# Optimization experiments

Hardware: AMD Instinct MI355X
Metric: run time of the kernel (lower is better)

## Reference

```python
import jax, jax.numpy as jnp
import numpy as np

B, C, N1 = 8, 1, 255
C_HID = 8
N2 = 2 * (N1 + 1)          # 512: antisymmetric expansion size
CROP = 2 * (N2 // 4) + 1   # 257: spectral crop size


def _expand(r):
    # odd antisymmetric extension to size 2*(M+1) x 2*(N+1)
    b, c, m, n = r.shape
    rsym = jnp.zeros((b, c, 2 * (m + 1), 2 * (n + 1)), r.dtype)
    rsym = rsym.at[:, :, 1:m + 1, 1:n + 1].set(r)
    rsym = rsym.at[:, :, m + 2:, 1:n + 1].set(-r[:, :, ::-1, :])
    rsym = rsym.at[:, :, 1:m + 1, n + 2:].set(-r[:, :, :, ::-1])
    rsym = rsym.at[:, :, m + 2:, n + 2:].set(r[:, :, ::-1, ::-1])
    return rsym


def _per_sample_conv(x, w):
    # Per-sample 3x3 cross-correlation, padding=1.
    # Equivalent to the torch module's F.conv2d over flattened [B*Cout,Cin,3,3]
    # followed by batch-diagonal extraction (without the O(B) wasted cross terms).
    # x: [B, Cin, H, W] complex; w: [B, Cout, Cin, 3, 3] complex.
    h, wd = x.shape[-2], x.shape[-1]
    xp = jnp.pad(x, ((0, 0), (0, 0), (1, 1), (1, 1)))
    out = 0.
    for di in range(3):
        for dj in range(3):
            out = out + jnp.einsum('bchw,boc->bohw', xp[:, :, di:di + h, dj:dj + wd], w[:, :, :, di, dj])
    return out


def _wT(w):
    # torch: transpose(-4,-3).transpose(-2,-1).conj() on [B,Cout,Cin,kh,kw]
    return jnp.conj(jnp.swapaxes(jnp.swapaxes(w, 1, 2), -2, -1))


def _forward(r, w1, w2, w3, theta):
    n1 = r.shape[-1]
    rsym = _expand(r)
    n2 = rsym.shape[-1]
    pl = n2 // 4 + 1
    pr = n2 - n2 // 2 - pl
    rh = jnp.fft.fftshift(jnp.fft.ifft2(rsym, axes=(2, 3)), axes=(2, 3))
    lo, hi = n2 // 2 - n2 // 4, n2 // 2 + n2 // 4 + 1
    rh = rh[:, :, lo:hi, lo:hi]                     # [B, C, CROP, CROP] complex
    for w in (w1, w2, w3):
        rh = _per_sample_conv(rh, w)
    out = rh * theta                                # spectral diagonal multiply
    for w in (_wT(w3), _wT(w2), _wT(w1)):
        out = _per_sample_conv(out, w)
    out = jnp.pad(out, ((0, 0), (0, 0), (pl, pr), (pl, pr)))
    out = jnp.fft.ifftshift(out, axes=(2, 3))
    e = jnp.fft.fft2(out, axes=(2, 3))
    return e[:, :, :n1, :n1]


def setup_inputs():
    key = jax.random.key(0)
    ks = jax.random.split(key, 9)
    s = jnp.float32(0.1)
    return {
        'r': jax.random.normal(ks[0], (B, C, N1, N1), jnp.float32),
        'w1_re': s * jax.random.normal(ks[1], (B, C_HID, C, 3, 3), jnp.float32),
        'w1_im': s * jax.random.normal(ks[2], (B, C_HID, C, 3, 3), jnp.float32),
        'w2_re': s * jax.random.normal(ks[3], (B, C_HID, C_HID, 3, 3), jnp.float32),
        'w2_im': s * jax.random.normal(ks[4], (B, C_HID, C_HID, 3, 3), jnp.float32),
        'w3_re': s * jax.random.normal(ks[5], (B, C_HID, C_HID, 3, 3), jnp.float32),
        'w3_im': s * jax.random.normal(ks[6], (B, C_HID, C_HID, 3, 3), jnp.float32),
        'theta_re': s * jax.random.normal(ks[7], (B, C_HID, CROP, CROP), jnp.float32),
        'theta_im': s * jax.random.normal(ks[8], (B, C_HID, CROP, CROP), jnp.float32),
    }


def reference(r, w1_re, w1_im, w2_re, w2_im, w3_re, w3_im, theta_re, theta_im):
    w1 = w1_re + 1j * w1_im
    w2 = w2_re + 1j * w2_im
    w3 = w3_re + 1j * w3_im
    theta = theta_re + 1j * theta_im
    return _forward(r, w1, w2, w3, theta)
```

## Files before the change

kernel.cpp:

```cpp
#include <hip/hip_runtime.h>

#define NB 8
#define CH 8
#define N1S 255
#define CROP 257
#define NOUT 255
#define CC (CROP * CROP)

static constexpr float PI2 = 6.28318530717958647692f;

__device__ inline unsigned short f2bf(float f) {
  unsigned int u = __float_as_uint(f);
  unsigned int lsb = (u >> 16) & 1u;
  u += 0x7fffu + lsb;
  return (unsigned short)(u >> 16);
}

__global__ void k_fill(unsigned short* __restrict__ out, int n, float v) {
  int i = blockIdx.x * 256 + threadIdx.x;
  if (i < n) out[i] = f2bf(v);
}

__global__ void k_tables(float* __restrict__ T, float* __restrict__ Tt,
                         float2* __restrict__ D, float2* __restrict__ Dt) {
  int idx = blockIdx.x * blockDim.x + threadIdx.x;
  if (idx < CROP * N1S) {
    int a = idx / N1S, p = idx % N1S;
    int v = (p + 1) * (a - 128);
    int t = v % 512; if (t < 0) t += 512; if (t >= 256) t -= 512;
    float s = sinf((float)t * (PI2 / 512.0f));
    T[a * N1S + p] = s;
    Tt[p * CROP + a] = s;
  }
  if (idx < NOUT * CROP) {
    int k = idx / CROP, j = idx % CROP;
    int v = k * (j - 127);
    int t = v % 513; if (t < 0) t += 513; if (t > 256) t -= 513;
    float ang = (float)t * (PI2 / 513.0f);
    float2 d = make_float2(cosf(ang), -sinf(ang));
    D[k * CROP + j] = d;
    Dt[j * NOUT + k] = d;
  }
}

__global__ void k_wprep(const float* __restrict__ w1re, const float* __restrict__ w1im,
                        const float* __restrict__ w2re, const float* __restrict__ w2im,
                        const float* __restrict__ w3re, const float* __restrict__ w3im,
                        float* __restrict__ wp) {
  int p = blockIdx.x * 256 + threadIdx.x;
  if (p >= 19584) return;
  int l, off;
  if      (p < 576)   { l = 0; off = 0; }
  else if (p < 5184)  { l = 1; off = 576; }
  else if (p < 9792)  { l = 2; off = 5184; }
  else if (p < 14400) { l = 3; off = 9792; }
  else if (p < 19008) { l = 4; off = 14400; }
  else                { l = 5; off = 19008; }
  int q = p - off;
  int cin  = (l == 0) ? 1 : 8;
  int cout = (l == 5) ? 1 : 8;
  int per_b = cin * cout * 9;
  int b = q / per_b, rem = q % per_b;
  int c = rem / (cout * 9), rem2 = rem % (cout * 9);
  int o = rem2 / 9, t9 = rem2 % 9;
  int di = t9 / 3, dj = t9 % 3;
  const float *wre, *wim;
  if (l == 0 || l == 5) { wre = w1re; wim = w1im; }
  else if (l == 1 || l == 4) { wre = w2re; wim = w2im; }
  else { wre = w3re; wim = w3im; }
  bool trans = (l >= 3);
  float wr, wi;
  if (trans) {
    int widx = (((b * cin + c) * cout + o) * 3 + dj) * 3 + di;
    wr = wre[widx]; wi = -wim[widx];
  } else {
    int widx = (((b * cout + o) * cin + c) * 3 + di) * 3 + dj;
    wr = wre[widx]; wi = wim[widx];
  }
  wp[2 * p] = wr;
  wp[2 * p + 1] = wi;
}


__global__ __launch_bounds__(512) void k_dst1(const float* __restrict__ r,
                                              const float* __restrict__ T,
                                              float* __restrict__ tmp) {
  __shared__ float As[32][16];
  __shared__ float Bs[16][64];
  const int tx = threadIdx.x, ty = threadIdx.y;
  const int tid = ty * 64 + tx;
  const int b = blockIdx.z;
  const int n = blockIdx.x * 64 + tx;
  const int a_base = blockIdx.y * 32;
  const float* rb = r + (size_t)b * N1S * N1S;
  float acc[4] = {};
  for (int mc = 0; mc < N1S; mc += 16) {
    { int row = tid / 16, col = tid % 16;
      int a = a_base + row, m = mc + col;
      As[row][col] = (a < CROP && m < N1S) ? T[a * N1S + m] : 0.f; }
    { int row = tid / 64, col = tid % 64;
      #pragma unroll
      for (int rr = 0; rr < 2; ++rr) {
        int m = mc + row + rr * 8, nn = blockIdx.x * 64 + col;
        Bs[row + rr * 8][col] = (m < N1S && nn < N1S) ? rb[m * N1S + nn] : 0.f;
      } }
    __syncthreads();
    #pragma unroll
    for (int jj = 0; jj < 16; ++jj) {
      float x = Bs[jj][tx];
      #pragma unroll
      for (int q = 0; q < 4; ++q)
        acc[q] = fmaf(As[ty * 4 + q][jj], x, acc[q]);
    }
    __syncthreads();
  }
  if (n < N1S) {
    #pragma unroll
    for (int q = 0; q < 4; ++q) {
      int a = a_base + ty * 4 + q;
      if (a < CROP) tmp[((size_t)b * CROP + a) * N1S + n] = acc[q];
    }
  }
}

__global__ __launch_bounds__(512) void k_dst2(const float* __restrict__ tmp,
                                              const float* __restrict__ Tt,
                                              float2* __restrict__ z0) {
  __shared__ float As[32][16];
  __shared__ float Bs[16][64];
  const int tx = threadIdx.x, ty = threadIdx.y;
  const int tid = ty * 64 + tx;
  const int b = blockIdx.z;
  const int a2 = blockIdx.x * 64 + tx;
  const int a_base = blockIdx.y * 32;
  const float* tb = tmp + (size_t)b * CROP * N1S;
  float acc[4] = {};
  for (int nc = 0; nc < N1S; nc += 16) {
    { int row = tid / 16, col = tid % 16;
      int a1 = a_base + row, nn = nc + col;
      As[row][col] = (a1 < CROP && nn < N1S) ? tb[a1 * N1S + nn] : 0.f; }
    { int row = tid / 64, col = tid % 64;
      #pragma unroll
      for (int rr = 0; rr < 2; ++rr) {
        int nn = nc + row + rr * 8, aa2 = blockIdx.x * 64 + col;
        Bs[row + rr * 8][col] = (nn < N1S && aa2 < CROP) ? Tt[nn * CROP + aa2] : 0.f;
      } }
    __syncthreads();
    #pragma unroll
    for (int jj = 0; jj < 16; ++jj) {
      float x = Bs[jj][tx];
      #pragma unroll
      for (int q = 0; q < 4; ++q)
        acc[q] = fmaf(As[ty * 4 + q][jj], x, acc[q]);
    }
    __syncthreads();
  }
  if (a2 < CROP) {
    #pragma unroll
    for (int q = 0; q < 4; ++q) {
      int a1 = a_base + ty * 4 + q;
      if (a1 < CROP)
        z0[((size_t)b * CROP + a1) * CROP + a2] = make_float2(acc[q] * (-1.0f / 65536.0f), 0.f);
    }
  }
}

__global__ __launch_bounds__(512) void k_f1(const float2* __restrict__ z,
                                            const float2* __restrict__ D,
                                            float2* __restrict__ t) {
  __shared__ float2 As[32][16];
  __shared__ float2 Bs[16][64];
  const int tx = threadIdx.x, ty = threadIdx.y;
  const int tid = ty * 64 + tx;
  const int b = blockIdx.z;
  const int j2 = blockIdx.x * 64 + tx;
  const int k_base = blockIdx.y * 32;
  const float2* zb = z + (size_t)b * CC;
  float tr[4] = {}, ti[4] = {};
  for (int jc = 0; jc < CROP; jc += 16) {
    { int row = tid / 16, col = tid % 16;
      int k = k_base + row, j1 = jc + col;
      As[row][col] = (k < NOUT && j1 < CROP) ? D[k * CROP + j1] : make_float2(0.f, 0.f); }
    { int row = tid / 64, col = tid % 64;
      #pragma unroll
      for (int rr = 0; rr < 2; ++rr) {
        int j1 = jc + row + rr * 8, jj2 = blockIdx.x * 64 + col;
        Bs[row + rr * 8][col] = (j1 < CROP && jj2 < CROP) ? zb[j1 * CROP + jj2] : make_float2(0.f, 0.f);
      } }
    __syncthreads();
    #pragma unroll
    for (int jj = 0; jj < 16; ++jj) {
      float2 zv = Bs[jj][tx];
      #pragma unroll
      for (int q = 0; q < 4; ++q) {
        float2 d = As[ty * 4 + q][jj];
        tr[q] = fmaf(d.x, zv.x, tr[q]); tr[q] = fmaf(-d.y, zv.y, tr[q]);
        ti[q] = fmaf(d.x, zv.y, ti[q]); ti[q] = fmaf(d.y, zv.x, ti[q]);
      }
    }
    __syncthreads();
  }
  if (j2 < CROP) {
    #pragma unroll
    for (int q = 0; q < 4; ++q) {
      int k = k_base + ty * 4 + q;
      if (k < NOUT)
        t[((size_t)b * NOUT + k) * CROP + j2] = make_float2(tr[q], ti[q]);
    }
  }
}

__global__ __launch_bounds__(512) void k_f2(const float2* __restrict__ t,
                                            const float2* __restrict__ Dt,
                                            ushort2* __restrict__ out) {
  __shared__ float2 As[32][16];
  __shared__ float2 Bs[16][64];
  const int tx = threadIdx.x, ty = threadIdx.y;
  const int tid = ty * 64 + tx;
  const int b = blockIdx.z;
  const int k2 = blockIdx.x * 64 + tx;
  const int k_base = blockIdx.y * 32;
  const float2* tb = t + (size_t)b * NOUT * CROP;
  float er[4] = {}, ei[4] = {};
  for (int jc = 0; jc < CROP; jc += 16) {
    { int row = tid / 16, col = tid % 16;
      int k1 = k_base + row, j = jc + col;
      As[row][col] = (k1 < NOUT && j < CROP) ? tb[k1 * CROP + j] : make_float2(0.f, 0.f); }
    { int row = tid / 64, col = tid % 64;
      #pragma unroll
      for (int rr = 0; rr < 2; ++rr) {
        int j = jc + row + rr * 8, kk2 = blockIdx.x * 64 + col;
        Bs[row + rr * 8][col] = (j < CROP && kk2 < NOUT) ? Dt[j * NOUT + kk2] : make_float2(0.f, 0.f);
      } }
    __syncthreads();
    #pragma unroll
    for (int jj = 0; jj < 16; ++jj) {
      float2 dv = Bs[jj][tx];
      #pragma unroll
      for (int q = 0; q < 4; ++q) {
        float2 tv = As[ty * 4 + q][jj];
        er[q] = fmaf(tv.x, dv.x, er[q]); er[q] = fmaf(-tv.y, dv.y, er[q]);
        ei[q] = fmaf(tv.x, dv.y, ei[q]); ei[q] = fmaf(tv.y, dv.x, ei[q]);
      }
    }
    __syncthreads();
  }
  if (k2 < NOUT) {
    #pragma unroll
    for (int q = 0; q < 4; ++q) {
      int k1 = k_base + ty * 4 + q;
      if (k1 < NOUT)
        out[((size_t)b * NOUT + k1) * NOUT + k2] = make_ushort2(f2bf(ei[q]), f2bf(er[q]));
    }
  }
}

template<int CIN, int COUT, bool THETA, bool REALIN>
__global__ __launch_bounds__(256) void k_conv(const float2* __restrict__ in,
                                              const float* __restrict__ wl,
                                              const float* __restrict__ tre,
                                              const float* __restrict__ tim,
                                              float2* __restrict__ out) {
  __shared__ float2 tile[CIN][18][18];
  const int b = blockIdx.z;
  const int tx = threadIdx.x, ty = threadIdx.y;
  const int tid = ty * 16 + tx;
  const int ox0 = blockIdx.x * 16, oy0 = blockIdx.y * 16;

  const float2* inb = in + (size_t)b * CIN * CC;
  for (int c = 0; c < CIN; ++c) {
    for (int idx = tid; idx < 18 * 18; idx += 256) {
      int iy = idx / 18, ix = idx % 18;
      int gy = oy0 + iy - 1, gx = ox0 + ix - 1;
      float2 v = make_float2(0.f, 0.f);
      if (gy >= 0 && gy < CROP && gx >= 0 && gx < CROP)
        v = inb[(c * CROP + gy) * CROP + gx];
      tile[c][iy][ix] = v;
    }
  }
  __syncthreads();
  const int ox = ox0 + tx, oy = oy0 + ty;
  if (ox >= CROP || oy >= CROP) return;
  float accr[COUT], acci[COUT];
  #pragma unroll
  for (int o = 0; o < COUT; ++o) { accr[o] = 0.f; acci[o] = 0.f; }
  #pragma unroll 1
  for (int c = 0; c < CIN; ++c) {
    const float* wsc = wl + (size_t)2 * ((b * CIN + c) * COUT * 9);
    float xr[9], xi[9];
    #pragma unroll
    for (int t9 = 0; t9 < 9; ++t9) {
      float2 v = tile[c][ty + t9 / 3][tx + t9 % 3];
      xr[t9] = v.x; if (!REALIN) xi[t9] = v.y;
    }
    #pragma unroll
    for (int o = 0; o < COUT; ++o) {
      #pragma unroll
      for (int t9 = 0; t9 < 9; ++t9) {
        float wr = wsc[(o * 9 + t9) * 2];
        float wi = wsc[(o * 9 + t9) * 2 + 1];
        if (REALIN) {
          accr[o] = fmaf(wr, xr[t9], accr[o]);
          acci[o] = fmaf(wi, xr[t9], acci[o]);
        } else {
          accr[o] = fmaf(wr, xr[t9], accr[o]);
          accr[o] = fmaf(-wi, xi[t9], accr[o]);
          acci[o] = fmaf(wr, xi[t9], acci[o]);
          acci[o] = fmaf(wi, xr[t9], acci[o]);
        }
      }
    }
  }
  float2* outb = out + (size_t)b * COUT * CC;
  #pragma unroll
  for (int o = 0; o < COUT; ++o) {
    float orv = accr[o], oiv = acci[o];
    if (THETA) {
      size_t tix = ((size_t)(b * COUT + o) * CROP + oy) * CROP + ox;
      float trv = tre[tix], tiv = tim[tix];
      float nr = orv * trv - oiv * tiv;
      float ni = orv * tiv + oiv * trv;
      orv = nr; oiv = ni;
    }
    outb[(o * CROP + oy) * CROP + ox] = make_float2(orv, oiv);
  }
}

extern "C" void kernel_launch(void* const* d_in, const int* in_sizes, int n_in,
                              void* d_out, int out_size, void* d_ws, size_t ws_size,
                              hipStream_t stream) {
  (void)ws_size;
  static const int EXP[9] = {520200, 576, 576, 4608, 4608, 4608, 4608, 4227136, 4227136};
  int bad = -1;
  if (n_in != 9) bad = 90;
  else for (int i = 0; i < 9; ++i) if (in_sizes[i] != EXP[i]) { bad = i; break; }
  if (bad >= 0) {
    float v = (bad == 90) ? 99.0f : (100.0f + (float)bad);
    k_fill<<<(out_size + 255) / 256, 256, 0, stream>>>((unsigned short*)d_out, out_size, v);
    return;
  }

  const float* r    = (const float*)d_in[0];
  const float* w1re = (const float*)d_in[1];
  const float* w1im = (const float*)d_in[2];
  const float* w2re = (const float*)d_in[3];
  const float* w2im = (const float*)d_in[4];
  const float* w3re = (const float*)d_in[5];
  const float* w3im = (const float*)d_in[6];
  const float* thre = (const float*)d_in[7];
  const float* thim = (const float*)d_in[8];

  float* ws = (float*)d_ws;
  size_t off = 0;
  auto alloc = [&](size_t n) { float* p = ws + off; off += (n + 63) & ~(size_t)63; return p; };
  float*  T    = alloc((size_t)CROP * N1S);
  float*  Tt   = alloc((size_t)N1S * CROP);
  float2* D    = (float2*)alloc((size_t)NOUT * CROP * 2);
  float2* Dt   = (float2*)alloc((size_t)CROP * NOUT * 2);
  float*  wp   = alloc((size_t)2 * 19584);
  float*  tmpA = alloc((size_t)NB * CROP * N1S);
  float2* z0   = (float2*)alloc((size_t)NB * CC * 2);
  float2* tmpF = (float2*)alloc((size_t)NB * NOUT * CROP * 2);
  float2* A    = (float2*)alloc((size_t)NB * CH * CC * 2);
  float2* Bb   = (float2*)alloc((size_t)NB * CH * CC * 2);

  k_tables<<<dim3((CROP * N1S + 255) / 256), dim3(256), 0, stream>>>(T, Tt, D, Dt);
  k_wprep<<<dim3(77), dim3(256), 0, stream>>>(w1re, w1im, w2re, w2im, w3re, w3im, wp);
  k_dst1<<<dim3(4, 9, NB), dim3(64, 8), 0, stream>>>(r, T, tmpA);
  k_dst2<<<dim3(5, 9, NB), dim3(64, 8), 0, stream>>>(tmpA, Tt, z0);

  dim3 cgrid(17, 17, NB), cblk(16, 16);
  k_conv<1, 8, false, true ><<<cgrid, cblk, 0, stream>>>(z0, wp + 2 * 0,     nullptr, nullptr, A);
  k_conv<8, 8, false, false><<<cgrid, cblk, 0, stream>>>(A,  wp + 2 * 576,   nullptr, nullptr, Bb);
  k_conv<8, 8, true , false><<<cgrid, cblk, 0, stream>>>(Bb, wp + 2 * 5184,  thre, thim, A);
  k_conv<8, 8, false, false><<<cgrid, cblk, 0, stream>>>(A,  wp + 2 * 9792,  nullptr, nullptr, Bb);
  k_conv<8, 8, false, false><<<cgrid, cblk, 0, stream>>>(Bb, wp + 2 * 14400, nullptr, nullptr, A);
  k_conv<8, 1, false, false><<<cgrid, cblk, 0, stream>>>(A,  wp + 2 * 19008, nullptr, nullptr, z0);

  k_f1<<<dim3(5, 8, NB), dim3(64, 8), 0, stream>>>(z0, D, tmpF);
  k_f2<<<dim3(4, 8, NB), dim3(64, 8), 0, stream>>>(tmpF, Dt, (ushort2*)d_out);
}
```

Measured before the change: 335.3 us.

## Fuse consecutive 3x3 complex convolutions pairwise with halo recompute in shared memory

Replaces six separate per-sample conv launches with three fused kernels, each running two 3x3 convolutions back to back. The intermediate 16x16 tile, which carries a one-pixel halo, stays in shared memory, and the theta multiply is applied between the two convs of the middle pair. This removes three global round-trips of the 8-channel complex intermediate and three launches. In exchange, each block now produces only 14x14 outputs, so halo work is recomputed and more blocks are launched. Shared memory use per block also goes up.

```diff
diff --git a/kernel.cpp b/kernel.cpp
--- a/kernel.cpp
+++ b/kernel.cpp
@@ -255,74 +255,115 @@
   }
 }
 
-template<int CIN, int COUT, bool THETA, bool REALIN>
-__global__ __launch_bounds__(256) void k_conv(const float2* __restrict__ in,
-                                              const float* __restrict__ wl,
-                                              const float* __restrict__ tre,
-                                              const float* __restrict__ tim,
-                                              float2* __restrict__ out) {
-  __shared__ float2 tile[CIN][18][18];
+template<int CIN, int COUT2, bool THETA_MID, bool REALIN>
+__global__ __launch_bounds__(256) void k_fused(const float2* __restrict__ in,
+                                               const float* __restrict__ wlA,
+                                               const float* __restrict__ wlB,
+                                               const float* __restrict__ tre,
+                                               const float* __restrict__ tim,
+                                               float2* __restrict__ out) {
+  __shared__ float2 tile1[CIN][18][18];
+  __shared__ float2 mid[8][16][17];
   const int b = blockIdx.z;
   const int tx = threadIdx.x, ty = threadIdx.y;
   const int tid = ty * 16 + tx;
-  const int ox0 = blockIdx.x * 16, oy0 = blockIdx.y * 16;
+  const int ox0 = blockIdx.x * 14, oy0 = blockIdx.y * 14;
 
   const float2* inb = in + (size_t)b * CIN * CC;
-  for (int c = 0; c < CIN; ++c) {
-    for (int idx = tid; idx < 18 * 18; idx += 256) {
-      int iy = idx / 18, ix = idx % 18;
-      int gy = oy0 + iy - 1, gx = ox0 + ix - 1;
-      float2 v = make_float2(0.f, 0.f);
-      if (gy >= 0 && gy < CROP && gx >= 0 && gx < CROP)
-        v = inb[(c * CROP + gy) * CROP + gx];
-      tile[c][iy][ix] = v;
-    }
+  #pragma unroll 1
+  for (int idx = tid; idx < CIN * 18 * 18; idx += 256) {
+    int c = idx / (18 * 18), rem = idx % (18 * 18);
+    int iy = rem / 18, ix = rem % 18;
+    int gy = oy0 + iy - 2, gx = ox0 + ix - 2;
+    float2 v = make_float2(0.f, 0.f);
+    if (gy >= 0 && gy < CROP && gx >= 0 && gx < CROP)
+      v = inb[(c * CROP + gy) * CROP + gx];
+    tile1[c][iy][ix] = v;
   }
   __syncthreads();
-  const int ox = ox0 + tx, oy = oy0 + ty;
-  if (ox >= CROP || oy >= CROP) return;
-  float accr[COUT], acci[COUT];
-  #pragma unroll
-  for (int o = 0; o < COUT; ++o) { accr[o] = 0.f; acci[o] = 0.f; }
-  #pragma unroll 1
-  for (int c = 0; c < CIN; ++c) {
-    const float* wsc = wl + (size_t)2 * ((b * CIN + c) * COUT * 9);
-    float xr[9], xi[9];
-    #pragma unroll
-    for (int t9 = 0; t9 < 9; ++t9) {
-      float2 v = tile[c][ty + t9 / 3][tx + t9 % 3];
-      xr[t9] = v.x; if (!REALIN) xi[t9] = v.y;
-    }
-    #pragma unroll
-    for (int o = 0; o < COUT; ++o) {
+
+  {
+    const int gmy = oy0 - 1 + ty, gmx = ox0 - 1 + tx;
+    const bool inside = (gmy >= 0 && gmy < CROP && gmx >= 0 && gmx < CROP);
+    float ar[8], ai[8];
+    #pragma unroll
+    for (int o = 0; o < 8; ++o) { ar[o] = 0.f; ai[o] = 0.f; }
+    #pragma unroll 1
+    for (int c = 0; c < CIN; ++c) {
+      const float* wsc = wlA + (size_t)2 * ((b * CIN + c) * 8 * 9);
+      float xr[9], xi[9];
       #pragma unroll
       for (int t9 = 0; t9 < 9; ++t9) {
-        float wr = wsc[(o * 9 + t9) * 2];
-        float wi = wsc[(o * 9 + t9) * 2 + 1];
-        if (REALIN) {
-          accr[o] = fmaf(wr, xr[t9], accr[o]);
-          acci[o] = fmaf(wi, xr[t9], acci[o]);
-        } else {
-          accr[o] = fmaf(wr, xr[t9], accr[o]);
-          accr[o] = fmaf(-wi, xi[t9], accr[o]);
-          acci[o] = fmaf(wr, xi[t9], acci[o]);
-          acci[o] = fmaf(wi, xr[t9], acci[o]);
+        float2 v = tile1[c][ty + t9 / 3][tx + t9 % 3];
+        xr[t9] = v.x; if (!REALIN) xi[t9] = v.y;
+      }
+      #pragma unroll
+      for (int o = 0; o < 8; ++o) {
+        #pragma unroll
+        for (int t9 = 0; t9 < 9; ++t9) {
+          float wr = wsc[(o * 9 + t9) * 2];
+          float wi = wsc[(o * 9 + t9) * 2 + 1];
+          if (REALIN) {
+            ar[o] = fmaf(wr, xr[t9], ar[o]);
+            ai[o] = fmaf(wi, xr[t9], ai[o]);
+          } else {
+            ar[o] = fmaf(wr, xr[t9], ar[o]);
+            ar[o] = fmaf(-wi, xi[t9], ar[o]);
+            ai[o] = fmaf(wr, xi[t9], ai[o]);
+            ai[o] = fmaf(wi, xr[t9], ai[o]);
+          }
         }
       }
     }
-  }
-  float2* outb = out + (size_t)b * COUT * CC;
-  #pragma unroll
-  for (int o = 0; o < COUT; ++o) {
-    float orv = accr[o], oiv = acci[o];
-    if (THETA) {
-      size_t tix = ((size_t)(b * COUT + o) * CROP + oy) * CROP + ox;
-      float trv = tre[tix], tiv = tim[tix];
-      float nr = orv * trv - oiv * tiv;
-      float ni = orv * tiv + oiv * trv;
-      orv = nr; oiv = ni;
-    }
-    outb[(o * CROP + oy) * CROP + ox] = make_float2(orv, oiv);
+    #pragma unroll
+    for (int o = 0; o < 8; ++o) {
+      float rv = ar[o], iv = ai[o];
+      if (THETA_MID) {
+        if (inside) {
+          size_t tix = ((size_t)(b * 8 + o) * CROP + gmy) * CROP + gmx;
+          float trv = tre[tix], tiv = tim[tix];
+          float nr = rv * trv - iv * tiv, ni = rv * tiv + iv * trv;
+          rv = nr; iv = ni;
+        }
+      }
+      mid[o][ty][tx] = inside ? make_float2(rv, iv) : make_float2(0.f, 0.f);
+    }
+  }
+  __syncthreads();
+
+  if (tx < 14 && ty < 14) {
+    const int oy = oy0 + ty, ox = ox0 + tx;
+    if (oy < CROP && ox < CROP) {
+      float ar[COUT2], ai[COUT2];
+      #pragma unroll
+      for (int o = 0; o < COUT2; ++o) { ar[o] = 0.f; ai[o] = 0.f; }
+      #pragma unroll 1
+      for (int c = 0; c < 8; ++c) {
+        const float* wsc = wlB + (size_t)2 * ((b * 8 + c) * COUT2 * 9);
+        float xr[9], xi[9];
+        #pragma unroll
+        for (int t9 = 0; t9 < 9; ++t9) {
+          float2 v = mid[c][ty + t9 / 3][tx + t9 % 3];
+          xr[t9] = v.x; xi[t9] = v.y;
+        }
+        #pragma unroll
+        for (int o = 0; o < COUT2; ++o) {
+          #pragma unroll
+          for (int t9 = 0; t9 < 9; ++t9) {
+            float wr = wsc[(o * 9 + t9) * 2];
+            float wi = wsc[(o * 9 + t9) * 2 + 1];
+            ar[o] = fmaf(wr, xr[t9], ar[o]);
+            ar[o] = fmaf(-wi, xi[t9], ar[o]);
+            ai[o] = fmaf(wr, xi[t9], ai[o]);
+            ai[o] = fmaf(wi, xr[t9], ai[o]);
+          }
+        }
+      }
+      float2* outb = out + (size_t)b * COUT2 * CC;
+      #pragma unroll
+      for (int o = 0; o < COUT2; ++o)
+        outb[(o * CROP + oy) * CROP + ox] = make_float2(ar[o], ai[o]);
+    }
   }
 }
 
@@ -369,13 +410,10 @@
   k_dst1<<<dim3(4, 9, NB), dim3(64, 8), 0, stream>>>(r, T, tmpA);
   k_dst2<<<dim3(5, 9, NB), dim3(64, 8), 0, stream>>>(tmpA, Tt, z0);
 
-  dim3 cgrid(17, 17, NB), cblk(16, 16);
-  k_conv<1, 8, false, true ><<<cgrid, cblk, 0, stream>>>(z0, wp + 2 * 0,     nullptr, nullptr, A);
-  k_conv<8, 8, false, false><<<cgrid, cblk, 0, stream>>>(A,  wp + 2 * 576,   nullptr, nullptr, Bb);
-  k_conv<8, 8, true , false><<<cgrid, cblk, 0, stream>>>(Bb, wp + 2 * 5184,  thre, thim, A);
-  k_conv<8, 8, false, false><<<cgrid, cblk, 0, stream>>>(A,  wp + 2 * 9792,  nullptr, nullptr, Bb);
-  k_conv<8, 8, false, false><<<cgrid, cblk, 0, stream>>>(Bb, wp + 2 * 14400, nullptr, nullptr, A);
-  k_conv<8, 1, false, false><<<cgrid, cblk, 0, stream>>>(A,  wp + 2 * 19008, nullptr, nullptr, z0);
+  dim3 fgrid(19, 19, NB), fblk(16, 16);
+  k_fused<1, 8, false, true ><<<fgrid, fblk, 0, stream>>>(z0, wp + 2 * 0,     wp + 2 * 576,   nullptr, nullptr, A);
+  k_fused<8, 8, true , false><<<fgrid, fblk, 0, stream>>>(A,  wp + 2 * 5184,  wp + 2 * 9792,  thre, thim, Bb);
+  k_fused<8, 1, false, false><<<fgrid, fblk, 0, stream>>>(Bb, wp + 2 * 14400, wp + 2 * 19008, nullptr, nullptr, z0);
 
   k_f1<<<dim3(5, 8, NB), dim3(64, 8), 0, stream>>>(z0, D, tmpF);
   k_f2<<<dim3(4, 8, NB), dim3(64, 8), 0, stream>>>(tmpF, Dt, (ushort2*)d_out);
```

Measured after the change: 313.0 us. 6.7% less time.
